# Performance work log

Hardware: AMD Instinct MI355X
Metric: run time of the kernel (lower is better)

## Reference

```python
import jax, jax.numpy as jnp
import numpy as np

D = 256      # embed_dim
H = 2        # num_heads
DH = D // H  # head_dim = 128
NL = 4       # number of MHA layers
L = 4096     # num faces (queries)
S = 8192     # num edges (keys/values)
E_LOOP = 32  # edges per face loop


def setup_inputs() -> dict:
    key = jax.random.key(0)
    ks = jax.random.split(key, 8)
    v_face_edge_loop = jax.random.randint(ks[0], (L, E_LOOP), 0, S, dtype=jnp.int64)
    v_face_mask = jnp.ones((L,), dtype=bool)
    v_edge_embedding = jax.random.normal(ks[1], (S, D), dtype=jnp.float32)
    v_face_embedding = jax.random.normal(ks[2], (L, D), dtype=jnp.float32)
    # per-layer MHA params, stacked along a leading layer dim (PyTorch layout: W [out,in])
    sc = 1.0 / np.sqrt(D)
    in_proj_w = jax.random.normal(ks[3], (NL, 3 * D, D), dtype=jnp.float32) * sc
    in_proj_b = jnp.zeros((NL, 3 * D), dtype=jnp.float32)
    out_proj_w = jax.random.normal(ks[4], (NL, D, D), dtype=jnp.float32) * sc
    out_proj_b = jnp.zeros((NL, D), dtype=jnp.float32)
    return {
        "v_face_edge_loop": v_face_edge_loop,
        "v_face_mask": v_face_mask,
        "v_edge_embedding": v_edge_embedding,
        "v_face_embedding": v_face_embedding,
        "in_proj_w": in_proj_w,
        "in_proj_b": in_proj_b,
        "out_proj_w": out_proj_w,
        "out_proj_b": out_proj_b,
    }


def _build_mask(loop, face_mask, n_edges):
    # rows with face_mask==False contribute no scatter (mapped to sentinel col S, trimmed)
    rel = jnp.where(face_mask[:, None], loop, -1)
    valid = (rel != -1) & (rel != -2)
    rel = jnp.where(valid, rel, n_edges)  # invalid -> overflow column
    n_faces = loop.shape[0]
    m = jnp.zeros((n_faces, n_edges + 1), dtype=bool)
    m = m.at[jnp.arange(n_faces)[:, None], rel].set(True)
    return m[:, :n_edges]  # [L, S]; True = NOT allowed (PyTorch attn_mask semantics)


def _mha(x, kv, mask, wqkv, bqkv, wo, bo):
    wq, wk, wv = jnp.split(wqkv, 3, axis=0)
    bq, bk, bv = jnp.split(bqkv, 3, axis=0)
    q = (x @ wq.T + bq).reshape(-1, H, DH)    # [L,H,DH]
    k = (kv @ wk.T + bk).reshape(-1, H, DH)   # [S,H,DH]
    v = (kv @ wv.T + bv).reshape(-1, H, DH)   # [S,H,DH]
    scores = jnp.einsum('lhd,shd->hls', q, k) / np.float32(np.sqrt(DH))
    scores = jnp.where(mask[None, :, :], -jnp.inf, scores)
    attn = jax.nn.softmax(scores, axis=-1)
    out = jnp.einsum('hls,shd->lhd', attn, v).reshape(-1, D)
    return out @ wo.T + bo


def reference(v_face_edge_loop, v_face_mask, v_edge_embedding, v_face_embedding,
              in_proj_w, in_proj_b, out_proj_w, out_proj_b):
    n_edges = v_edge_embedding.shape[0]
    mask = _build_mask(v_face_edge_loop, v_face_mask, n_edges)
    x = v_face_embedding
    for i in range(NL):
        x = _mha(x, v_edge_embedding, mask,
                 in_proj_w[i], in_proj_b[i], out_proj_w[i], out_proj_b[i])
    return x
```

## Files before the change

kernel.cpp:

```cpp
#include <hip/hip_runtime.h>
#include <math.h>

typedef _Float16 f16;
typedef _Float16 f16x4 __attribute__((ext_vector_type(4)));
typedef _Float16 f16x8 __attribute__((ext_vector_type(8)));
typedef float f32x4 __attribute__((ext_vector_type(4)));
typedef float f32x16 __attribute__((ext_vector_type(16)));

#define MFMA_F16 __builtin_amdgcn_mfma_f32_16x16x32_f16
#define MFMA32_F16 __builtin_amdgcn_mfma_f32_32x32x16_f16

namespace {
constexpr int kL = 4096;
constexpr int kS = 8192;
constexpr int kD = 256;
constexpr int kH = 2;
constexpr int kDH = 128;
constexpr int kNL = 4;
constexpr int kNS = 8;
constexpr float kScale = 0.08838834764831845f;
}

__global__ __launch_bounds__(256) void cvt_all_k(
    const float* __restrict__ edge, const float* __restrict__ face,
    const float* __restrict__ inw, const float* __restrict__ outw,
    f16* __restrict__ e16, f16* __restrict__ xa,
    f16* __restrict__ win16, f16* __restrict__ wout16) {
  for (int i = blockIdx.x * 256 + threadIdx.x; i < 1048576; i += 1024 * 256) {
    const float* src;
    f16* dst;
    int off;
    if (i < 524288) { src = edge; dst = e16; off = i; }
    else if (i < 786432) { src = face; dst = xa; off = i - 524288; }
    else if (i < 983040) { src = inw; dst = win16; off = i - 786432; }
    else { src = outw; dst = wout16; off = i - 983040; }
    float4 v = *(const float4*)(src + 4 * (size_t)off);
    f16x4 h;
    h[0] = (f16)v.x; h[1] = (f16)v.y; h[2] = (f16)v.z; h[3] = (f16)v.w;
    *(f16x4*)(dst + 4 * (size_t)off) = h;
  }
}

__global__ __launch_bounds__(256) void detect_k(const unsigned int* __restrict__ loopw,
                                                const unsigned char* __restrict__ maskb,
                                                int* __restrict__ flags) {
  __shared__ unsigned int s[3];
  if (threadIdx.x < 3) s[threadIdx.x] = 0;
  __syncthreads();
  unsigned int orodd = 0;
  for (int i = 1 + 2 * threadIdx.x; i < 2048; i += 512) orodd |= loopw[i];
  unsigned int nz1 = 0, nz4 = 0;
  for (int i = threadIdx.x; i < 512; i += 256) {
    unsigned char b = maskb[i];
    if ((i & 3) != 0) nz1 |= b;
    if ((i & 7) == 4) nz4 |= b;
  }
  atomicOr(&s[0], orodd);
  atomicOr(&s[1], nz1);
  atomicOr(&s[2], nz4);
  __syncthreads();
  if (threadIdx.x == 0) {
    flags[0] = (s[0] == 0) ? 2 : 1;
    flags[1] = s[1] ? 1 : (s[2] ? 4 : 8);
  }
}

__device__ __forceinline__ void gemm_core(const f16* __restrict__ A,
                                          const f16* __restrict__ W, int K,
                                          int m0, int n0, int r, int g,
                                          f32x4 acc[2][2]) {
  const f16* ap0 = A + (size_t)(m0 + r) * K + g * 8;
  const f16* ap1 = ap0 + (size_t)16 * K;
  const f16* bp0 = W + (size_t)(n0 + r) * K + g * 8;
  const f16* bp1 = bp0 + (size_t)16 * K;
#pragma unroll 8
  for (int kc = 0; kc < K; kc += 32) {
    f16x8 a0 = *(const f16x8*)(ap0 + kc);
    f16x8 a1 = *(const f16x8*)(ap1 + kc);
    f16x8 b0 = *(const f16x8*)(bp0 + kc);
    f16x8 b1 = *(const f16x8*)(bp1 + kc);
    acc[0][0] = MFMA_F16(a0, b0, acc[0][0], 0, 0, 0);
    acc[0][1] = MFMA_F16(a0, b1, acc[0][1], 0, 0, 0);
    acc[1][0] = MFMA_F16(a1, b0, acc[1][0], 0, 0, 0);
    acc[1][1] = MFMA_F16(a1, b1, acc[1][1], 0, 0, 0);
  }
}

__global__ __launch_bounds__(256) void qkv_gemm_k(
    const f16* __restrict__ x, const f16* __restrict__ e16,
    const f16* __restrict__ wql, const float* __restrict__ biasl,
    f16* __restrict__ q16, f16* __restrict__ k16,
    f16* __restrict__ vt16, f16* __restrict__ v16) {
  __shared__ __align__(16) f16 Tl[64][72];
  const int lane = threadIdx.x & 63;
  const int wid = threadIdx.x >> 6;
  const int r = lane & 15, g = lane >> 4;
  const int bid = blockIdx.x;
  const bool qmode = bid < 256;
  int bx, by;
  const f16* A;
  const f16* W;
  const float* bias;
  if (qmode) {
    bx = bid & 63; by = bid >> 6;
    A = x; W = wql; bias = biasl;
  } else {
    int t = bid - 256;
    bx = t & 127; by = t >> 7;
    A = e16; W = wql + (size_t)kD * kD; bias = biasl + kD;
  }
  const int m0 = bx * 64 + (wid >> 1) * 32;
  const int n0 = by * 64 + (wid & 1) * 32;
  const bool vmode = !qmode && (by >= 4);
  f32x4 acc[2][2] = {};
  gemm_core(A, W, kD, m0, n0, r, g, acc);

#pragma unroll
  for (int mt = 0; mt < 2; ++mt)
#pragma unroll
    for (int nt = 0; nt < 2; ++nt) {
      int col = n0 + nt * 16 + r;
      float bv = bias[col];
#pragma unroll
      for (int i = 0; i < 4; ++i) {
        int row = m0 + mt * 16 + g * 4 + i;
        float v = acc[mt][nt][i] + bv;
        if (qmode) {
          q16[(size_t)row * kD + col] = (f16)v;
        } else if (!vmode) {
          k16[(size_t)row * 256 + col] = (f16)v;
        } else {
          int dv = col - 256;
          v16[(size_t)row * 256 + dv] = (f16)v;
          int nl = (wid & 1) * 32 + nt * 16 + r;
          int rl = (wid >> 1) * 32 + mt * 16 + g * 4 + i;
          Tl[nl][rl] = (f16)v;
        }
      }
    }
  if (vmode) {
    __syncthreads();
    const int dvb = (by - 4) * 64;
    const int key0 = bx * 64;
#pragma unroll
    for (int it = 0; it < 2; ++it) {
      int rowd = it * 32 + (threadIdx.x >> 3);
      int seg = (threadIdx.x & 7) * 8;
      *(f16x8*)&vt16[(size_t)(dvb + rowd) * kS + key0 + seg] =
          *(const f16x8*)&Tl[rowd][seg];
    }
  }
}

__global__ __launch_bounds__(256) void gemm_awt_k(
    const f16* __restrict__ A, const f16* __restrict__ W,
    const float* __restrict__ bias, f16* __restrict__ C16,
    float* __restrict__ C32, int M, int N, int K) {
  const int lane = threadIdx.x & 63;
  const int wid = threadIdx.x >> 6;
  const int r = lane & 15, g = lane >> 4;
  const int m0 = blockIdx.x * 64 + (wid >> 1) * 32;
  const int n0 = blockIdx.y * 64 + (wid & 1) * 32;
  f32x4 acc[2][2] = {};
  gemm_core(A, W, K, m0, n0, r, g, acc);
#pragma unroll
  for (int mt = 0; mt < 2; ++mt)
#pragma unroll
    for (int nt = 0; nt < 2; ++nt) {
      int col = n0 + nt * 16 + r;
      float bv = bias[col];
#pragma unroll
      for (int i = 0; i < 4; ++i) {
        int row = m0 + mt * 16 + g * 4 + i;
        float v = acc[mt][nt][i] + bv;
        C16[(size_t)row * N + col] = (f16)v;
        if (C32) C32[(size_t)row * N + col] = v;
      }
    }
}

__device__ __forceinline__ unsigned pkh(float a, float b) {
  auto h2 = __builtin_amdgcn_cvt_pkrtz(a, b);
  return __builtin_bit_cast(unsigned, h2);
}
__device__ __forceinline__ void pswap(unsigned a, unsigned b, unsigned& x,
                                      unsigned& y) {
  typedef int i32x2 __attribute__((ext_vector_type(2)));
  i32x2 rr = __builtin_amdgcn_permlane32_swap((int)a, (int)b, false, false);
  x = (unsigned)rr[0];
  y = (unsigned)rr[1];
}
__device__ __forceinline__ f16x8 build_pfrag(float p0, float p1, float p2,
                                             float p3, float p4, float p5,
                                             float p6, float p7) {
  unsigned a0 = pkh(p0, p1), b0 = pkh(p4, p5);
  unsigned a1 = pkh(p2, p3), b1 = pkh(p6, p7);
  unsigned w0, w1, w2, w3;
  pswap(a0, b0, w0, w2);
  pswap(a1, b1, w1, w3);
  union { unsigned u[4]; f16x8 v; } r;
  r.u[0] = w0; r.u[1] = w1; r.u[2] = w2; r.u[3] = w3;
  return r.v;
}

__global__ __launch_bounds__(256, 2) void attn_dense7_k(
    const f16* __restrict__ Q, const f16* __restrict__ Km,
    const f16* __restrict__ Vt,
    f16* __restrict__ numOut, float* __restrict__ denOut) {
  __shared__ __align__(16) f16 Kl[2][64 * 128];
  __shared__ __align__(16) f16 Vl[2][128 * 64];
  const int tid = threadIdx.x;
  const int lane = tid & 63, wid = tid >> 6;
  const int la = lane & 31, hi = lane >> 5;
  const int id = blockIdx.x;
  const int grp = id & 15;
  const int h = grp & 1;
  const int z = grp >> 1;
  const int bx = id >> 4;
  const int q0w = bx * 128 + wid * 32;
  const int sb0 = z * (kS / kNS);
  const int nt = (kS / kNS) / 64;

  f16x8 qb[8];
#pragma unroll
  for (int kk = 0; kk < 8; ++kk)
    qb[kk] = *(const f16x8*)(Q + (size_t)(q0w + la) * kD + h * kDH + kk * 16 +
                             hi * 8);

  int kSrc[4], kDst[4], vSrc[4], vDst[4];
#pragma unroll
  for (int p = 0; p < 4; ++p) {
    int m = wid * 16 + p * 4 + (lane >> 4);
    int s = lane & 15;
    kSrc[p] = (sb0 + m) * kD + h * kDH + 8 * (s ^ (m & 7));
    kDst[p] = m * 128 + 8 * s;
    int cv = p * 256 + tid;
    int d = cv >> 3, sv = cv & 7;
    vSrc[p] = (h * kDH + d) * kS + sb0 + 8 * (sv ^ (d & 7));
    vDst[p] = d * 64 + 8 * sv;
  }

  f32x16 o0 = {}, o1 = {}, o2 = {}, o3 = {};
  float den = 0.0f;
  f16x8 kst[4], vst[4];

#pragma unroll
  for (int p = 0; p < 4; ++p) {
    kst[p] = *(const f16x8*)(Km + kSrc[p]);
    vst[p] = *(const f16x8*)(Vt + vSrc[p]);
  }
#pragma unroll
  for (int p = 0; p < 4; ++p) {
    *(f16x8*)&Kl[0][kDst[p]] = kst[p];
    *(f16x8*)&Vl[0][vDst[p]] = vst[p];
  }
  __syncthreads();

  for (int t = 0; t < nt; ++t) {
    const int cur = t & 1;
    if (t + 1 < nt) {
#pragma unroll
      for (int p = 0; p < 4; ++p) {
        kst[p] = *(const f16x8*)(Km + kSrc[p] + (t + 1) * 64 * kD);
        vst[p] = *(const f16x8*)(Vt + vSrc[p] + (t + 1) * 64);
      }
    }

    f32x16 st0 = {}, st1 = {};
    __builtin_amdgcn_s_setprio(1);
#pragma unroll
    for (int kk = 0; kk < 8; ++kk) {
      int sl = 8 * ((kk * 2 + hi) ^ (la & 7));
      f16x8 k0 = *(const f16x8*)&Kl[cur][la * 128 + sl];
      f16x8 k1 = *(const f16x8*)&Kl[cur][(32 + la) * 128 + sl];
      st0 = MFMA32_F16(k0, qb[kk], st0, 0, 0, 0);
      st1 = MFMA32_F16(k1, qb[kk], st1, 0, 0, 0);
    }
    __builtin_amdgcn_s_setprio(0);

    f32x16 pe0, pe1;
#pragma unroll
    for (int i = 0; i < 16; ++i) {
      pe0[i] = __expf(st0[i] * kScale);
      pe1[i] = __expf(st1[i] * kScale);
    }
#pragma unroll
    for (int i = 0; i < 16; ++i) den += pe0[i] + pe1[i];

    f16x8 pf[4];
    pf[0] = build_pfrag(pe0[0], pe0[1], pe0[2], pe0[3], pe0[4], pe0[5], pe0[6], pe0[7]);
    pf[1] = build_pfrag(pe0[8], pe0[9], pe0[10], pe0[11], pe0[12], pe0[13], pe0[14], pe0[15]);
    pf[2] = build_pfrag(pe1[0], pe1[1], pe1[2], pe1[3], pe1[4], pe1[5], pe1[6], pe1[7]);
    pf[3] = build_pfrag(pe1[8], pe1[9], pe1[10], pe1[11], pe1[12], pe1[13], pe1[14], pe1[15]);

    __builtin_amdgcn_s_setprio(1);
#pragma unroll
    for (int dt = 0; dt < 4; ++dt) {
      int d = dt * 32 + la;
      f32x16* op = (dt == 0) ? &o0 : (dt == 1) ? &o1 : (dt == 2) ? &o2 : &o3;
#pragma unroll
      for (int ks = 0; ks < 4; ++ks) {
        f16x8 vf = *(const f16x8*)&Vl[cur][d * 64 + 8 * ((ks * 2 + hi) ^ (d & 7))];
        *op = MFMA32_F16(vf, pf[ks], *op, 0, 0, 0);
      }
    }
    __builtin_amdgcn_s_setprio(0);

    if (t + 1 < nt) {
      const int nxt = cur ^ 1;
#pragma unroll
      for (int p = 0; p < 4; ++p) {
        *(f16x8*)&Kl[nxt][kDst[p]] = kst[p];
        *(f16x8*)&Vl[nxt][vDst[p]] = vst[p];
      }
      __syncthreads();
    }
  }

  const size_t nbase = ((size_t)z * kH + h) * kL + q0w;
  const size_t rowb = (nbase + la) * kDH;
#pragma unroll
  for (int dt = 0; dt < 4; ++dt) {
    const f32x16* op = (dt == 0) ? &o0 : (dt == 1) ? &o1 : (dt == 2) ? &o2 : &o3;
    unsigned u01 = pkh((*op)[0], (*op)[1]);
    unsigned u23 = pkh((*op)[2], (*op)[3]);
    unsigned u89 = pkh((*op)[4], (*op)[5]);
    unsigned uab = pkh((*op)[6], (*op)[7]);
    unsigned w0, w1, w2, w3;
    pswap(u01, u89, w0, w2);
    pswap(u23, uab, w1, w3);
    union { unsigned u[4]; f16x8 v; } r1;
    r1.u[0] = w0; r1.u[1] = w1; r1.u[2] = w2; r1.u[3] = w3;
    *(f16x8*)&numOut[rowb + dt * 32 + hi * 8] = r1.v;

    unsigned v01 = pkh((*op)[8], (*op)[9]);
    unsigned v23 = pkh((*op)[10], (*op)[11]);
    unsigned v89 = pkh((*op)[12], (*op)[13]);
    unsigned vab = pkh((*op)[14], (*op)[15]);
    unsigned x0, x1, x2, x3;
    pswap(v01, v89, x0, x2);
    pswap(v23, vab, x1, x3);
    union { unsigned u[4]; f16x8 v; } r2;
    r2.u[0] = x0; r2.u[1] = x1; r2.u[2] = x2; r2.u[3] = x3;
    *(f16x8*)&numOut[rowb + dt * 32 + 16 + hi * 8] = r2.v;
  }
  float dq = den + __shfl_xor(den, 32);
  if (lane < 32)
    denOut[((size_t)z * kH + h) * kL + q0w + lane] = dq;
}

__global__ __launch_bounds__(256) void corrcomb_k(
    const unsigned int* __restrict__ loopw, const unsigned char* __restrict__ maskb,
    const int* __restrict__ flags,
    const f16* __restrict__ Q, const f16* __restrict__ Km,
    const f16* __restrict__ V,
    const f16* __restrict__ numb, const float* __restrict__ denb,
    f16* __restrict__ out16) {
  __shared__ float cvL[4][128];
  __shared__ float csL[4];
  const int lane = threadIdx.x & 63;
  const int wid = threadIdx.x >> 6;
  const int w = blockIdx.x * 4 + wid;
  const int f = w >> 1, h = w & 1;
  const int lstride = flags[0];
  const int mstride = flags[1];

  int idx = -1, valid = 0;
  if (lane < 32) {
    idx = (int)loopw[(size_t)(f * 32 + lane) * lstride];
    valid = maskb[(size_t)f * mstride] ? 1 : 0;
  }
#pragma unroll
  for (int j = 0; j < 32; ++j) {
    int oidx = __shfl(idx, j);
    if (lane < 32 && j < lane && oidx == idx) valid = 0;
  }

  const size_t qb = (size_t)f * kD + h * kDH + 2 * lane;
  const float qa = (float)Q[qb];
  const float qbv = (float)Q[qb + 1];
  float s0 = 0.0f, cv0 = 0.0f, cv1 = 0.0f;
  for (int e = 0; e < 32; ++e) {
    int ei = __shfl(idx, e);
    int ev = __shfl(valid, e);
    if (!ev) continue;
    size_t kb = (size_t)ei * kD + h * kDH + 2 * lane;
    float part = qa * (float)Km[kb] + qbv * (float)Km[kb + 1];
#pragma unroll
    for (int m = 1; m < 64; m <<= 1) part += __shfl_xor(part, m);
    float pe = __expf(part * kScale);
    s0 += pe;
    cv0 += pe * (float)V[kb];
    cv1 += pe * (float)V[kb + 1];
  }
  cvL[wid][2 * lane] = cv0;
  cvL[wid][2 * lane + 1] = cv1;
  if (lane == 0) csL[wid] = s0;
  __syncthreads();

#pragma unroll
  for (int e = 0; e < 2; ++e) {
    int idx2 = e * 256 + threadIdx.x;
    int floc = idx2 >> 8;
    int c = idx2 & 255;
    int h2 = c >> 7;
    int d = c & 127;
    int widx = floc * 2 + h2;
    int fabs_ = blockIdx.x * 2 + floc;
    float n = -cvL[widx][d];
    float dn = -csL[widx];
#pragma unroll
    for (int z = 0; z < kNS; ++z) {
      n += (float)numb[((size_t)(z * kH + h2) * kL + fabs_) * kDH + d];
      dn += denb[((size_t)z * kH + h2) * kL + fabs_];
    }
    out16[(size_t)fabs_ * kD + h2 * kDH + d] = (f16)(n / dn);
  }
}

extern "C" void kernel_launch(void* const* d_in, const int* in_sizes, int n_in,
                              void* d_out, int out_size, void* d_ws, size_t ws_size,
                              hipStream_t stream) {
  const unsigned int* loopw = (const unsigned int*)d_in[0];
  const unsigned char* fmask = (const unsigned char*)d_in[1];
  const float* edge = (const float*)d_in[2];
  const float* face = (const float*)d_in[3];
  const float* inw = (const float*)d_in[4];
  const float* inb = (const float*)d_in[5];
  const float* outw = (const float*)d_in[6];
  const float* outb = (const float*)d_in[7];
  float* out = (float*)d_out;

  char* p = (char*)d_ws;
  auto alloc = [&](size_t bytes) {
    char* q = p;
    p += (bytes + 255) & ~(size_t)255;
    return q;
  };
  int* flags = (int*)alloc(256);
  f16* e16 = (f16*)alloc((size_t)kS * kD * 2);
  f16* win16 = (f16*)alloc((size_t)kNL * 3 * kD * kD * 2);
  f16* wout16 = (f16*)alloc((size_t)kNL * kD * kD * 2);
  f16* xa = (f16*)alloc((size_t)kL * kD * 2);
  f16* xb = (f16*)alloc((size_t)kL * kD * 2);
  f16* q16 = (f16*)alloc((size_t)kL * kD * 2);
  f16* k16 = (f16*)alloc((size_t)kS * kD * 2);
  f16* v16 = (f16*)alloc((size_t)kS * kD * 2);
  f16* vt16 = (f16*)alloc((size_t)kS * kD * 2);
  f16* ao16 = (f16*)alloc((size_t)kL * kD * 2);
  f16* numb = (f16*)alloc((size_t)kNS * kH * kL * kDH * 2);
  float* denb = (float*)alloc((size_t)kNS * kH * kL * 4);

  detect_k<<<1, 256, 0, stream>>>(loopw, fmask, flags);
  cvt_all_k<<<1024, 256, 0, stream>>>(edge, face, inw, outw, e16, xa, win16,
                                      wout16);

  f16* x = xa;
  f16* xn = xb;
  for (int l = 0; l < kNL; ++l) {
    const f16* wql = win16 + (size_t)l * 3 * kD * kD;
    qkv_gemm_k<<<1280, 256, 0, stream>>>(x, e16, wql, inb + l * 3 * kD, q16,
                                         k16, vt16, v16);
    attn_dense7_k<<<512, 256, 0, stream>>>(q16, k16, vt16, numb, denb);
    corrcomb_k<<<kL / 2, 256, 0, stream>>>(loopw, fmask, flags, q16, k16, v16,
                                           numb, denb, ao16);
    gemm_awt_k<<<dim3(kL / 64, kD / 64), 256, 0, stream>>>(
        ao16, wout16 + (size_t)l * kD * kD, outb + l * kD, xn,
        (l == kNL - 1) ? out : nullptr, kL, kD, kD);
    f16* tmp = x;
    x = xn;
    xn = tmp;
  }
}
```

Measured before the change: 419.5 us.

## Fold out-projection into next layer's Q projection and precompute all-layer K/V

```diff
diff --git a/kernel.cpp b/kernel.cpp
--- a/kernel.cpp
+++ b/kernel.cpp
@@ -63,6 +63,31 @@
     flags[0] = (s[0] == 0) ? 2 : 1;
     flags[1] = s[1] ? 1 : (s[2] ? 4 : 8);
   }
+}
+
+__global__ __launch_bounds__(256) void compose_k(
+    const float* __restrict__ inw, const float* __restrict__ inb,
+    const float* __restrict__ outw, const float* __restrict__ outb,
+    f16* __restrict__ wqo, float* __restrict__ bprime) {
+  const int lc = blockIdx.y;
+  const int i = blockIdx.x;
+  const int j = threadIdx.x;
+  const int l = lc + 1;
+  const float* wq = inw + (size_t)l * 3 * kD * kD;
+  const float* wo = outw + (size_t)lc * kD * kD;
+  float acc = 0.0f;
+  for (int k = 0; k < kD; ++k)
+    acc += wq[i * kD + k] * wo[k * kD + j];
+  wqo[((size_t)lc * kD + i) * kD + j] = (f16)acc;
+
+  float t = wq[i * kD + j] * outb[lc * kD + j];
+  __shared__ float red[4];
+#pragma unroll
+  for (int m = 1; m < 64; m <<= 1) t += __shfl_xor(t, m);
+  if ((threadIdx.x & 63) == 0) red[threadIdx.x >> 6] = t;
+  __syncthreads();
+  if (threadIdx.x == 0)
+    bprime[lc * kD + i] = red[0] + red[1] + red[2] + red[3] + inb[l * 3 * kD + i];
 }
 
 __device__ __forceinline__ void gemm_core(const f16* __restrict__ A,
@@ -86,34 +111,30 @@
   }
 }
 
-__global__ __launch_bounds__(256) void qkv_gemm_k(
-    const f16* __restrict__ x, const f16* __restrict__ e16,
-    const f16* __restrict__ wql, const float* __restrict__ biasl,
-    f16* __restrict__ q16, f16* __restrict__ k16,
-    f16* __restrict__ vt16, f16* __restrict__ v16) {
+__global__ __launch_bounds__(256) void kvall_gemm_k(
+    const f16* __restrict__ e16, const f16* __restrict__ win16,
+    const float* __restrict__ inb,
+    f16* __restrict__ k16all, f16* __restrict__ vt16all,
+    f16* __restrict__ v16all) {
   __shared__ __align__(16) f16 Tl[64][72];
   const int lane = threadIdx.x & 63;
   const int wid = threadIdx.x >> 6;
   const int r = lane & 15, g = lane >> 4;
   const int bid = blockIdx.x;
-  const bool qmode = bid < 256;
-  int bx, by;
-  const f16* A;
-  const f16* W;
-  const float* bias;
-  if (qmode) {
-    bx = bid & 63; by = bid >> 6;
-    A = x; W = wql; bias = biasl;
-  } else {
-    int t = bid - 256;
-    bx = t & 127; by = t >> 7;
-    A = e16; W = wql + (size_t)kD * kD; bias = biasl + kD;
-  }
+  const int l = bid >> 10;
+  const int t = bid & 1023;
+  const int bx = t & 127, by = t >> 7;
+  const f16* W = win16 + (size_t)l * 3 * kD * kD + (size_t)kD * kD;
+  const float* bias = inb + l * 3 * kD + kD;
+  f16* k16 = k16all + (size_t)l * kS * kD;
+  f16* vt16 = vt16all + (size_t)l * kS * kD;
+  f16* v16 = v16all + (size_t)l * kS * kD;
+
   const int m0 = bx * 64 + (wid >> 1) * 32;
   const int n0 = by * 64 + (wid & 1) * 32;
-  const bool vmode = !qmode && (by >= 4);
+  const bool vmode = (by >= 4);
   f32x4 acc[2][2] = {};
-  gemm_core(A, W, kD, m0, n0, r, g, acc);
+  gemm_core(e16, W, kD, m0, n0, r, g, acc);
 
 #pragma unroll
   for (int mt = 0; mt < 2; ++mt)
@@ -125,9 +146,7 @@
       for (int i = 0; i < 4; ++i) {
         int row = m0 + mt * 16 + g * 4 + i;
         float v = acc[mt][nt][i] + bv;
-        if (qmode) {
-          q16[(size_t)row * kD + col] = (f16)v;
-        } else if (!vmode) {
+        if (!vmode) {
           k16[(size_t)row * 256 + col] = (f16)v;
         } else {
           int dv = col - 256;
@@ -442,33 +461,42 @@
   f16* win16 = (f16*)alloc((size_t)kNL * 3 * kD * kD * 2);
   f16* wout16 = (f16*)alloc((size_t)kNL * kD * kD * 2);
   f16* xa = (f16*)alloc((size_t)kL * kD * 2);
-  f16* xb = (f16*)alloc((size_t)kL * kD * 2);
   f16* q16 = (f16*)alloc((size_t)kL * kD * 2);
-  f16* k16 = (f16*)alloc((size_t)kS * kD * 2);
-  f16* v16 = (f16*)alloc((size_t)kS * kD * 2);
-  f16* vt16 = (f16*)alloc((size_t)kS * kD * 2);
   f16* ao16 = (f16*)alloc((size_t)kL * kD * 2);
+  f16* scr16 = (f16*)alloc((size_t)kL * kD * 2);
+  f16* wqo = (f16*)alloc((size_t)3 * kD * kD * 2);
+  float* bprime = (float*)alloc((size_t)3 * kD * 4);
+  f16* k16all = (f16*)alloc((size_t)kNL * kS * kD * 2);
+  f16* vt16all = (f16*)alloc((size_t)kNL * kS * kD * 2);
+  f16* v16all = (f16*)alloc((size_t)kNL * kS * kD * 2);
   f16* numb = (f16*)alloc((size_t)kNS * kH * kL * kDH * 2);
   float* denb = (float*)alloc((size_t)kNS * kH * kL * 4);
 
   detect_k<<<1, 256, 0, stream>>>(loopw, fmask, flags);
   cvt_all_k<<<1024, 256, 0, stream>>>(edge, face, inw, outw, e16, xa, win16,
                                       wout16);
-
-  f16* x = xa;
-  f16* xn = xb;
+  compose_k<<<dim3(256, 3), 256, 0, stream>>>(inw, inb, outw, outb, wqo,
+                                              bprime);
+  kvall_gemm_k<<<4096, 256, 0, stream>>>(e16, win16, inb, k16all, vt16all,
+                                         v16all);
+
   for (int l = 0; l < kNL; ++l) {
-    const f16* wql = win16 + (size_t)l * 3 * kD * kD;
-    qkv_gemm_k<<<1280, 256, 0, stream>>>(x, e16, wql, inb + l * 3 * kD, q16,
-                                         k16, vt16, v16);
-    attn_dense7_k<<<512, 256, 0, stream>>>(q16, k16, vt16, numb, denb);
-    corrcomb_k<<<kL / 2, 256, 0, stream>>>(loopw, fmask, flags, q16, k16, v16,
+    const f16* kl = k16all + (size_t)l * kS * kD;
+    const f16* vtl = vt16all + (size_t)l * kS * kD;
+    const f16* vl = v16all + (size_t)l * kS * kD;
+    if (l == 0) {
+      gemm_awt_k<<<dim3(64, 4), 256, 0, stream>>>(
+          xa, win16, inb, q16, nullptr, kL, kD, kD);
+    } else {
+      gemm_awt_k<<<dim3(64, 4), 256, 0, stream>>>(
+          ao16, wqo + (size_t)(l - 1) * kD * kD, bprime + (l - 1) * kD, q16,
+          nullptr, kL, kD, kD);
+    }
+    attn_dense7_k<<<512, 256, 0, stream>>>(q16, kl, vtl, numb, denb);
+    corrcomb_k<<<kL / 2, 256, 0, stream>>>(loopw, fmask, flags, q16, kl, vl,
                                            numb, denb, ao16);
-    gemm_awt_k<<<dim3(kL / 64, kD / 64), 256, 0, stream>>>(
-        ao16, wout16 + (size_t)l * kD * kD, outb + l * kD, xn,
-        (l == kNL - 1) ? out : nullptr, kL, kD, kD);
-    f16* tmp = x;
-    x = xn;
-    xn = tmp;
-  }
-}
+  }
+  gemm_awt_k<<<dim3(64, 4), 256, 0, stream>>>(
+      ao16, wout16 + (size_t)3 * kD * kD, outb + 3 * kD, scr16, out, kL, kD,
+      kD);
+}
```

After: 411.6 us. No clear change (-1.9%).
